# Kernel tuning notes

Measured on AMD Instinct MI355X. Metric: run time of the kernel, lower is better.

Reference implementation:

```python
import jax, jax.numpy as jnp
import numpy as np
from math import sqrt

NUM_HEADS = 16
DIM_MODEL = 1024


def setup_inputs() -> dict:
    key = jax.random.key(0)
    ks = jax.random.split(key, 12)
    B, S, D, M = 4, 1024, DIM_MODEL, 64
    bound = 1.0 / sqrt(D)
    def lin_w(k):
        return jax.random.uniform(k, (D, D), jnp.float32, -bound, bound)
    def lin_b(k):
        return jax.random.uniform(k, (D,), jnp.float32, -bound, bound)
    return {
        "query": jax.random.normal(ks[0], (B, S, D), jnp.float32),
        "key": jax.random.normal(ks[1], (B, S, D), jnp.float32),
        "value": jax.random.normal(ks[2], (B, S, D), jnp.float32),
        "mask": jax.random.randint(ks[3], (1, B, S, M), 0, 2).astype(jnp.float32),
        "Wq": lin_w(ks[4]), "bq": lin_b(ks[5]),
        "Wk": lin_w(ks[6]), "bk": lin_b(ks[7]),
        "Wv": lin_w(ks[8]), "bv": lin_b(ks[9]),
        "Wo": lin_w(ks[10]),
    }


def reference(query, key, value, mask, Wq, bq, Wk, bk, Wv, bv, Wo):
    B, S, D = query.shape
    H = NUM_HEADS
    d = D // H
    # projections + head split, permute(2,0,1,3) -> [H,B,S,d]
    q = (query @ Wq.T + bq).reshape(B, S, H, d).transpose(2, 0, 1, 3)
    k = (key @ Wk.T + bk).reshape(B, S, H, d).transpose(2, 0, 1, 3)
    v = (value @ Wv.T + bv).reshape(B, S, H, d).transpose(2, 0, 1, 3)
    attn = jnp.einsum("hbqd,hbkd->hbqk", q, k) / sqrt(d)  # [H,B,S,S]
    # custom mask: mask.repeat(H,1,1,1) then mask @ mask^T / sqrt(m).
    # Identical per-head, so compute once on [B,S,m] and broadcast over H.
    m2d = mask[0]  # [B,S,m]
    mm = jnp.einsum("bqm,bkm->bqk", m2d, m2d) / sqrt(m2d.shape[-1])
    attn = jnp.where(mm[None] == 0, jnp.float32(-1e9), attn)
    w = jax.nn.softmax(attn, axis=-1)  # dropout is identity in eval mode
    x = jnp.einsum("hbqk,hbkd->hbqd", w, v)  # [H,B,S,d]
    # torch: permute(1,2,0,3) -> [B,S,H,d]; transpose(1,2) -> [B,H,S,d];
    # contiguous().view(B,-1,H*d) -- row-major reshape (mixes head/seq layout, replicated faithfully)
    x = jnp.transpose(x, (1, 0, 2, 3))  # [B,H,S,d]
    x = x.reshape(B, -1, H * d)
    return x @ Wo.T
```

## Files before the change

### kernel.cpp

```cpp
#include <hip/hip_runtime.h>

typedef unsigned int u32;
typedef unsigned short u16;
typedef unsigned long long u64;
typedef __attribute__((ext_vector_type(8))) short s16x8;
typedef __attribute__((ext_vector_type(8))) __bf16 bf16x8;
typedef __attribute__((ext_vector_type(4))) float f32x4;
typedef __attribute__((ext_vector_type(16))) float f32x16;
typedef __attribute__((ext_vector_type(4))) u32 u32x4;

#define WSMB (1ull << 20)
#define QSC 0.18033688011112042f

static __device__ __forceinline__ u16 f2bf(float f) {
  u32 u = __builtin_bit_cast(u32, f);
  return (u16)((u + 0x7fffu + ((u >> 16) & 1u)) >> 16);
}

static __device__ __forceinline__ u32 pkbf(float lo, float hi) {
  u32 r;
  asm("v_cvt_pk_bf16_f32 %0, %1, %2" : "=v"(r) : "v"(lo), "v"(hi));
  return r;
}

static __device__ __forceinline__ float ex2(float x) {
  float r;
  asm("v_exp_f32 %0, %1" : "=v"(r) : "v"(x));
  return r;
}

static __device__ __forceinline__ f32x4 mfma16x16(s16x8 a, s16x8 b, f32x4 c) {
  return __builtin_amdgcn_mfma_f32_16x16x32_bf16(
      __builtin_bit_cast(bf16x8, a), __builtin_bit_cast(bf16x8, b), c, 0, 0, 0);
}

static __device__ __forceinline__ f32x16 mfma32x32(s16x8 a, s16x8 b, f32x16 c) {
  return __builtin_amdgcn_mfma_f32_32x32x16_bf16(
      __builtin_bit_cast(bf16x8, a), __builtin_bit_cast(bf16x8, b), c, 0, 0, 0);
}

#define GLOAD_LDS16(g, l)                                                      \
  __builtin_amdgcn_global_load_lds(                                            \
      (const __attribute__((address_space(1))) u32*)(const void*)(g),          \
      (__attribute__((address_space(3))) u32*)(void*)(l), 16, 0, 0)

__global__ __launch_bounds__(256) void k_prep(
    const float* __restrict__ xq, const float* __restrict__ xk,
    const float* __restrict__ xv, const float* __restrict__ wq,
    const float* __restrict__ wk, const float* __restrict__ wv,
    const float* __restrict__ wo, const float* __restrict__ mask,
    u16* __restrict__ oxq, u16* __restrict__ oxk, u16* __restrict__ oxv,
    u16* __restrict__ owq, u16* __restrict__ owk, u16* __restrict__ owv,
    u16* __restrict__ owo, u64* __restrict__ bits) {
  const int y = blockIdx.y;
  if (y >= 3 && blockIdx.x >= 1024) return;
  if (y == 7) {
    int w = threadIdx.x >> 6, l = threadIdx.x & 63;
    int r = blockIdx.x * 4 + w;
    float v = mask[(size_t)r * 64 + l];
    u64 bl = __ballot(v != 0.0f);
    if (l == 0) bits[r] = bl;
    return;
  }
  const float* s;
  u16* d;
  switch (y) {
    case 0: s = xq; d = oxq; break;
    case 1: s = xk; d = oxk; break;
    case 2: s = xv; d = oxv; break;
    case 3: s = wq; d = owq; break;
    case 4: s = wk; d = owk; break;
    case 5: s = wv; d = owv; break;
    default: s = wo; d = owo; break;
  }
  int i = (blockIdx.x * 256 + threadIdx.x) * 4;
  float4 v = *(const float4*)(s + i);
  u64 p = (u64)f2bf(v.x) | ((u64)f2bf(v.y) << 16) | ((u64)f2bf(v.z) << 32) |
          ((u64)f2bf(v.w) << 48);
  *(u64*)(d + i) = p;
}

__global__ __launch_bounds__(256) void k_mm(const u64* __restrict__ bits,
                                            u64* __restrict__ MB) {
  int wv = threadIdx.x >> 6, l = threadIdx.x & 63;
  int qg = blockIdx.x * 4 + wv;
  u64 bq = bits[qg];
  const u64* bb = bits + (qg & ~1023);
  u64* out = MB + (size_t)qg * 16;
  for (int kt = 0; kt < 16; kt++) {
    u64 bk = bb[kt * 64 + l];
    u64 m = __ballot((bq & bk) != 0ull);
    if (l == 0) out[kt] = m;
  }
}

static __device__ __forceinline__ void gemm_core(const u16* __restrict__ A,
                                                 const u16* __restrict__ Bw,
                                                 f32x4 (&acc)[4][4]) {
  __shared__ __attribute__((aligned(16))) u16 As[2][4096];
  __shared__ __attribute__((aligned(16))) u16 Bs[2][4096];
  const int t = threadIdx.x;
  const int l = t & 63, w = t >> 6, lr = l & 15, lk = l >> 4;
  const int amr = (w & 1) * 64, bnr = (w >> 1) * 64;
  const int c0 = t, c1 = t + 256;
  const int r0 = c0 >> 2, r1 = c1 >> 2;
  const int sw0 = ((c0 & 3) * 8) ^ ((r0 & 6) << 2);
  const int sw1 = ((c1 & 3) * 8) ^ ((r1 & 6) << 2);
  const u16* Ag0 = A + (size_t)r0 * 1024 + sw0;
  const u16* Ag1 = A + (size_t)r1 * 1024 + sw1;
  const u16* Bg0 = Bw + (size_t)r0 * 1024 + sw0;
  const u16* Bg1 = Bw + (size_t)r1 * 1024 + sw1;
  const int aswz = (lk * 16) ^ ((lr & 6) << 3);

  GLOAD_LDS16(Ag0, &As[0][c0 * 8]);
  GLOAD_LDS16(Ag1, &As[0][c1 * 8]);
  GLOAD_LDS16(Bg0, &Bs[0][c0 * 8]);
  GLOAD_LDS16(Bg1, &Bs[0][c1 * 8]);

  int cur = 0;
  for (int kt = 0; kt < 1024; kt += 32) {
    __syncthreads();
    if (kt < 992) {
      const int nxt = cur ^ 1;
      GLOAD_LDS16(Ag0 + kt + 32, &As[nxt][c0 * 8]);
      GLOAD_LDS16(Ag1 + kt + 32, &As[nxt][c1 * 8]);
      GLOAD_LDS16(Bg0 + kt + 32, &Bs[nxt][c0 * 8]);
      GLOAD_LDS16(Bg1 + kt + 32, &Bs[nxt][c1 * 8]);
    }
    const char* Ac = (const char*)As[cur];
    const char* Bc = (const char*)Bs[cur];
    s16x8 af[4], bf[4];
#pragma unroll
    for (int i = 0; i < 4; i++)
      af[i] = *(const s16x8*)(Ac + (amr + i * 16 + lr) * 64 + aswz);
#pragma unroll
    for (int j = 0; j < 4; j++)
      bf[j] = *(const s16x8*)(Bc + (bnr + j * 16 + lr) * 64 + aswz);
    __builtin_amdgcn_s_setprio(1);
#pragma unroll
    for (int i = 0; i < 4; i++)
#pragma unroll
      for (int j = 0; j < 4; j++)
        acc[i][j] = mfma16x16(af[i], bf[j], acc[i][j]);
    __builtin_amdgcn_s_setprio(0);
    cur ^= 1;
  }
}

__global__ __launch_bounds__(256) void k_qkv(
    const u16* __restrict__ Xq, const u16* __restrict__ Xk,
    const u16* __restrict__ Xv, const u16* __restrict__ Wqb,
    const u16* __restrict__ Wkb, const u16* __restrict__ Wvb,
    const float* __restrict__ bq, const float* __restrict__ bk,
    const float* __restrict__ bv, u16* __restrict__ Qo, u16* __restrict__ Ko,
    u16* __restrict__ V4) {
  const int bid0 = blockIdx.x;
  const int bid = (bid0 & 7) * 96 + (bid0 >> 3);
  const int proj = bid >> 8;
  const int rem = bid & 255;
  const int st = rem >> 3, dt = rem & 7;
  const u16* Xp = proj == 0 ? Xq : (proj == 1 ? Xk : Xv);
  const u16* Wp = proj == 0 ? Wqb : (proj == 1 ? Wkb : Wvb);
  const float* bias = proj == 0 ? bq : (proj == 1 ? bk : bv);
  const int t = threadIdx.x;
  const int l = t & 63, w = t >> 6, lr = l & 15, lk = l >> 4;
  const int amr = (w & 1) * 64, bnr = (w >> 1) * 64;
  f32x4 acc[4][4] = {};
  if (proj < 2) {
    const float sc = proj == 0 ? QSC : 1.0f;
    gemm_core(Wp + (size_t)dt * 131072, Xp + (size_t)st * 131072, acc);
    u16* O = proj ? Ko : Qo;
#pragma unroll
    for (int i = 0; i < 4; i++) {
      const int d0 = dt * 128 + amr + i * 16 + lk * 4;
      const int h = d0 >> 6, dd0 = d0 & 63;
      const float4 b4 = *(const float4*)(bias + d0);
#pragma unroll
      for (int j = 0; j < 4; j++) {
        const int s = st * 128 + bnr + j * 16 + lr;
        const int b_ = s >> 10, si = s & 1023;
        u32 e0 = pkbf((acc[i][j][0] + b4.x) * sc, (acc[i][j][1] + b4.y) * sc);
        u32 e1 = pkbf((acc[i][j][2] + b4.z) * sc, (acc[i][j][3] + b4.w) * sc);
        *(u64*)(O + ((size_t)((b_ * 16 + h) * 1024 + si)) * 64 + dd0) =
            (u64)e0 | ((u64)e1 << 32);
      }
    }
  } else {
    gemm_core(Xp + (size_t)st * 131072, Wp + (size_t)dt * 131072, acc);
#pragma unroll
    for (int i = 0; i < 4; i++) {
      const int s0 = st * 128 + amr + i * 16 + lk * 4;
      const int b_ = s0 >> 10, si = s0 & 1023;
      const int sblk = si >> 3, soff = si & 7;
#pragma unroll
      for (int j = 0; j < 4; j++) {
        const int d = dt * 128 + bnr + j * 16 + lr;
        const int h = d >> 6, dd = d & 63;
        const float bb = bias[d];
        u32 e0 = pkbf(acc[i][j][0] + bb, acc[i][j][1] + bb);
        u32 e1 = pkbf(acc[i][j][2] + bb, acc[i][j][3] + bb);
        *(u64*)(V4 + (size_t)(b_ * 16 + h) * 65536 +
                (size_t)(sblk * 64 + dd) * 8 + soff) =
            (u64)e0 | ((u64)e1 << 32);
      }
    }
  }
}

__global__ __launch_bounds__(256) void k_oproj(const u16* __restrict__ Xb,
                                               const u16* __restrict__ Wob,
                                               float* __restrict__ Out) {
  const int bid0 = blockIdx.x;
  const int bid = (bid0 & 7) * 32 + (bid0 >> 3);
  const int mb = bid >> 3, nb = bid & 7;
  f32x4 acc[4][4] = {};
  gemm_core(Xb + (size_t)mb * 131072, Wob + (size_t)nb * 131072, acc);
  const int t = threadIdx.x;
  const int l = t & 63, w = t >> 6, lr = l & 15, lk = l >> 4;
  const int amr = (w & 1) * 64, bnr = (w >> 1) * 64;
#pragma unroll
  for (int i = 0; i < 4; i++)
#pragma unroll
    for (int j = 0; j < 4; j++)
#pragma unroll
      for (int r = 0; r < 4; r++) {
        const int m = mb * 128 + amr + i * 16 + lk * 4 + r;
        const int n = nb * 128 + bnr + j * 16 + lr;
        Out[(size_t)m * 1024 + n] = acc[i][j][r];
      }
}

__global__ __launch_bounds__(256, 3) void k_attn(const u16* __restrict__ Qb,
                                                 const u16* __restrict__ Kb,
                                                 const u16* __restrict__ V4,
                                                 const u64* __restrict__ MB,
                                                 u16* __restrict__ xbuf) {
  __shared__ __attribute__((aligned(16))) u16 Ks[2][4096];
  __shared__ __attribute__((aligned(16))) u16 Vs[2][4096];
  const int t = threadIdx.x, l = t & 63, w = t >> 6;
  const int q5 = l & 31, hi = l >> 5;
  const int bid = (blockIdx.x & 7) * 64 + (blockIdx.x >> 3);
  const int qt = bid & 7, hb = bid >> 3;
  const int h = hb >> 2, b = hb & 3;
  const int s0 = qt * 128;
  const u16* Qhb = Qb + (size_t)(b * 16 + h) * 65536;
  const u16* Khb = Kb + (size_t)(b * 16 + h) * 65536;
  const u16* Vhb = V4 + (size_t)(b * 16 + h) * 65536;
  const int q = s0 + w * 32 + q5;
  const u64* MBq = MB + ((size_t)b * 1024 + q) * 16;

  s16x8 qf[4];
#pragma unroll
  for (int ds = 0; ds < 4; ds++)
    qf[ds] = *(const s16x8*)(Qhb + (size_t)q * 64 + ds * 16 + hi * 8);

  f32x16 xa0 = {}, xa1 = {};
  float ls = 0.f, m_ = -__builtin_inff();

  const int ca = t, cb_ = t + 256;
  const int rA = ca >> 3, colA = (ca & 7) * 16;
  const int rB = cb_ >> 3, colB = (cb_ & 7) * 16;
  const int sA = colA ^ ((rA & 7) << 4);
  const int sB = colB ^ ((rB & 7) << 4);
  const u16* KgA = Khb + (size_t)rA * 64 + (sA >> 1);
  const u16* KgB = Khb + (size_t)rB * 64 + (sB >> 1);
  const u16* VgA = Vhb + (size_t)(sA >> 4) * 512 + rA * 8;
  const u16* VgB = Vhb + (size_t)(sB >> 4) * 512 + rB * 8;

  const int rbase = q5 * 128 + ((hi * 16) ^ ((q5 & 7) << 4));

  GLOAD_LDS16(KgA, &Ks[0][ca * 8]);
  GLOAD_LDS16(KgB, &Ks[0][cb_ * 8]);
  GLOAD_LDS16(VgA, &Vs[0][ca * 8]);
  GLOAD_LDS16(VgB, &Vs[0][cb_ * 8]);
  u64 mw = MBq[0];

  int cur = 0;
  for (int kt = 0; kt < 16; kt++) {
    __syncthreads();
    if (kt < 15) {
      const int nxt = cur ^ 1;
      GLOAD_LDS16(KgA + (kt + 1) * 4096, &Ks[nxt][ca * 8]);
      GLOAD_LDS16(KgB + (kt + 1) * 4096, &Ks[nxt][cb_ * 8]);
      GLOAD_LDS16(VgA + (kt + 1) * 4096, &Vs[nxt][ca * 8]);
      GLOAD_LDS16(VgB + (kt + 1) * 4096, &Vs[nxt][cb_ * 8]);
    }
    const u64 nw = MBq[(kt + 1) & 15];
    const char* Kc = (const char*)Ks[cur];
    const char* Vc = (const char*)Vs[cur];

    f32x16 z0 = {}, z1 = {};
#pragma unroll
    for (int ds = 0; ds < 4; ds++) {
      s16x8 k0 = *(const s16x8*)(Kc + (rbase ^ (ds * 32)));
      s16x8 k1 = *(const s16x8*)(Kc + 4096 + (rbase ^ (ds * 32)));
      __builtin_amdgcn_s_setprio(1);
      z0 = mfma32x32(k0, qf[ds], z0);
      z1 = mfma32x32(k1, qf[ds], z1);
      __builtin_amdgcn_s_setprio(0);
    }

    float tmx[16];
#pragma unroll
    for (int r = 0; r < 16; r++) tmx[r] = fmaxf(z0[r], z1[r]);
#pragma unroll
    for (int st_ = 8; st_ >= 1; st_ >>= 1)
#pragma unroll
      for (int r = 0; r < 8; r++)
        if (r < st_) tmx[r] = fmaxf(tmx[r], tmx[r + st_]);
    float tm = tmx[0];
    tm = fmaxf(tm, __shfl_xor(tm, 32));
    if (tm > m_) {
      const float scl = ex2(m_ - tm);
      m_ = tm;
      ls *= scl;
      xa0 *= scl;
      xa1 *= scl;
    }

    float e0[16], e1[16];
#pragma unroll
    for (int r = 0; r < 16; r++) e0[r] = ex2(z0[r] - m_);
#pragma unroll
    for (int r = 0; r < 16; r++) e1[r] = ex2(z1[r] - m_);
    if (!__all(mw == ~0ull)) {
      const u32 mh0 = (u32)(mw >> (hi * 4));
      const u32 mh1 = (u32)(mw >> (hi * 4 + 32));
#pragma unroll
      for (int r = 0; r < 16; r++) {
        const int bp = 8 * (r >> 2) + (r & 3);
        e0[r] = ((mh0 >> bp) & 1u) ? e0[r] : 0.f;
        e1[r] = ((mh1 >> bp) & 1u) ? e1[r] : 0.f;
      }
    }
    float ts = 0.f;
#pragma unroll
    for (int r = 0; r < 16; r++) ts += e0[r] + e1[r];
    ls += ts;

    u32 P0[2][4], P1[2][4];
#pragma unroll
    for (int qi = 0; qi < 4; qi++) {
      P0[0][qi] = pkbf(e0[4 * qi], e0[4 * qi + 1]);
      P1[0][qi] = pkbf(e0[4 * qi + 2], e0[4 * qi + 3]);
      P0[1][qi] = pkbf(e1[4 * qi], e1[4 * qi + 1]);
      P1[1][qi] = pkbf(e1[4 * qi + 2], e1[4 * qi + 3]);
    }

#pragma unroll
    for (int ks = 0; ks < 4; ks++) {
      const int kb = ks >> 1, qi0 = (ks & 1) * 2, qi1 = qi0 + 1;
      u32 w0 = P0[kb][qi0], w2 = P0[kb][qi1];
      u32 w1 = P1[kb][qi0], w3 = P1[kb][qi1];
      asm("v_permlane32_swap_b32 %0, %1" : "+v"(w0), "+v"(w2));
      asm("v_permlane32_swap_b32 %0, %1" : "+v"(w1), "+v"(w3));
      u32x4 fv;
      fv[0] = w0; fv[1] = w1; fv[2] = w2; fv[3] = w3;
      const s16x8 pb = __builtin_bit_cast(s16x8, fv);
      s16x8 v0 = *(const s16x8*)(Vc + (rbase ^ (ks * 32)));
      s16x8 v1 = *(const s16x8*)(Vc + 4096 + (rbase ^ (ks * 32)));
      __builtin_amdgcn_s_setprio(1);
      xa0 = mfma32x32(v0, pb, xa0);
      xa1 = mfma32x32(v1, pb, xa1);
      __builtin_amdgcn_s_setprio(0);
    }
    mw = nw;
    cur ^= 1;
  }

  ls += __shfl_xor(ls, 32);
  const float inv = 1.0f / ls;
  const size_t rowb = (size_t)b * 1048576 + (size_t)(h * 64 + (q >> 4)) * 1024 +
                      (size_t)(q & 15) * 64;
#pragma unroll
  for (int qi = 0; qi < 4; qi++) {
    u32 a0 = pkbf(xa0[4 * qi] * inv, xa0[4 * qi + 1] * inv);
    u32 a1 = pkbf(xa0[4 * qi + 2] * inv, xa0[4 * qi + 3] * inv);
    *(u64*)(xbuf + rowb + 8 * qi + 4 * hi) = (u64)a0 | ((u64)a1 << 32);
    u32 b0 = pkbf(xa1[4 * qi] * inv, xa1[4 * qi + 1] * inv);
    u32 b1 = pkbf(xa1[4 * qi + 2] * inv, xa1[4 * qi + 3] * inv);
    *(u64*)(xbuf + rowb + 32 + 8 * qi + 4 * hi) = (u64)b0 | ((u64)b1 << 32);
  }
}

extern "C" void kernel_launch(void* const* d_in, const int* in_sizes, int n_in,
                              void* d_out, int out_size, void* d_ws,
                              size_t ws_size, hipStream_t stream) {
  const float* query = (const float*)d_in[0];
  const float* key_ = (const float*)d_in[1];
  const float* value = (const float*)d_in[2];
  const float* mask = (const float*)d_in[3];
  const float* bq = (const float*)d_in[5];
  const float* bk = (const float*)d_in[7];
  const float* bv = (const float*)d_in[9];
  const float* Wq = (const float*)d_in[4];
  const float* Wk = (const float*)d_in[6];
  const float* Wv = (const float*)d_in[8];
  const float* Wo = (const float*)d_in[10];

  char* ws = (char*)d_ws;
  u16* Xq = (u16*)(ws + 0 * WSMB);
  u16* Xk = (u16*)(ws + 8 * WSMB);
  u16* Xv = (u16*)(ws + 16 * WSMB);
  u16* Wqb = (u16*)(ws + 24 * WSMB);
  u16* Wkb = (u16*)(ws + 26 * WSMB);
  u16* Wvb = (u16*)(ws + 28 * WSMB);
  u16* Wob = (u16*)(ws + 30 * WSMB);
  u16* Qb = (u16*)(ws + 32 * WSMB);
  u16* Kb = (u16*)(ws + 40 * WSMB);
  u16* V4 = (u16*)(ws + 48 * WSMB);
  u64* bits = (u64*)(ws + 56 * WSMB);
  u64* MBm = (u64*)(ws + 8 * WSMB);
  u16* xbuf = Xq;

  k_prep<<<dim3(4096, 8), 256, 0, stream>>>(query, key_, value, Wq, Wk, Wv, Wo,
                                            mask, Xq, Xk, Xv, Wqb, Wkb, Wvb,
                                            Wob, bits);
  k_qkv<<<768, 256, 0, stream>>>(Xq, Xk, Xv, Wqb, Wkb, Wvb, bq, bk, bv, Qb, Kb,
                                 V4);
  k_mm<<<1024, 256, 0, stream>>>(bits, MBm);
  k_attn<<<512, 256, 0, stream>>>(Qb, Kb, V4, MBm, xbuf);
  k_oproj<<<256, 256, 0, stream>>>(xbuf, Wob, (float*)d_out);
}
```

Measured before the change: 116.9 us.

## Flatten prep grid, fuse mask-matmul into QKV launch, halve oproj tile width

Replaces the 2D prep grid, which launched many blocks that exited immediately, with a flat 1D grid holding exactly the needed blocks. The mask-bit matmul kernel is folded into the QKV projection launch as extra blocks, which removes one launch and lets that work overlap the GEMM tail. Its output buffer moves to a separate workspace slot so it cannot collide with the bf16 X buffers still being read. The output projection uses 128x64 tiles instead of 128x128, doubling the block count to 512 for better CU occupancy, at the cost of reloading the A operand more often.

```diff
diff --git a/kernel.cpp b/kernel.cpp
--- a/kernel.cpp
+++ b/kernel.cpp
@@ -52,11 +52,10 @@
     u16* __restrict__ oxq, u16* __restrict__ oxk, u16* __restrict__ oxv,
     u16* __restrict__ owq, u16* __restrict__ owk, u16* __restrict__ owv,
     u16* __restrict__ owo, u64* __restrict__ bits) {
-  const int y = blockIdx.y;
-  if (y >= 3 && blockIdx.x >= 1024) return;
-  if (y == 7) {
+  const int bid = blockIdx.x;
+  if (bid >= 16384) {
     int w = threadIdx.x >> 6, l = threadIdx.x & 63;
-    int r = blockIdx.x * 4 + w;
+    int r = (bid - 16384) * 4 + w;
     float v = mask[(size_t)r * 64 + l];
     u64 bl = __ballot(v != 0.0f);
     if (l == 0) bits[r] = bl;
@@ -64,34 +63,26 @@
   }
   const float* s;
   u16* d;
-  switch (y) {
-    case 0: s = xq; d = oxq; break;
-    case 1: s = xk; d = oxk; break;
-    case 2: s = xv; d = oxv; break;
-    case 3: s = wq; d = owq; break;
-    case 4: s = wk; d = owk; break;
-    case 5: s = wv; d = owv; break;
-    default: s = wo; d = owo; break;
-  }
-  int i = (blockIdx.x * 256 + threadIdx.x) * 4;
+  int x;
+  if (bid < 12288) {
+    const int y = bid >> 12;
+    x = bid & 4095;
+    if (y == 0) { s = xq; d = oxq; }
+    else if (y == 1) { s = xk; d = oxk; }
+    else { s = xv; d = oxv; }
+  } else {
+    const int y = (bid - 12288) >> 10;
+    x = (bid - 12288) & 1023;
+    if (y == 0) { s = wq; d = owq; }
+    else if (y == 1) { s = wk; d = owk; }
+    else if (y == 2) { s = wv; d = owv; }
+    else { s = wo; d = owo; }
+  }
+  int i = (x * 256 + threadIdx.x) * 4;
   float4 v = *(const float4*)(s + i);
   u64 p = (u64)f2bf(v.x) | ((u64)f2bf(v.y) << 16) | ((u64)f2bf(v.z) << 32) |
           ((u64)f2bf(v.w) << 48);
   *(u64*)(d + i) = p;
-}
-
-__global__ __launch_bounds__(256) void k_mm(const u64* __restrict__ bits,
-                                            u64* __restrict__ MB) {
-  int wv = threadIdx.x >> 6, l = threadIdx.x & 63;
-  int qg = blockIdx.x * 4 + wv;
-  u64 bq = bits[qg];
-  const u64* bb = bits + (qg & ~1023);
-  u64* out = MB + (size_t)qg * 16;
-  for (int kt = 0; kt < 16; kt++) {
-    u64 bk = bb[kt * 64 + l];
-    u64 m = __ballot((bq & bk) != 0ull);
-    if (l == 0) out[kt] = m;
-  }
 }
 
 static __device__ __forceinline__ void gemm_core(const u16* __restrict__ A,
@@ -147,14 +138,78 @@
   }
 }
 
+static __device__ __forceinline__ void gemm_core64(const u16* __restrict__ A,
+                                                   const u16* __restrict__ Bw,
+                                                   f32x4 (&acc)[4][2]) {
+  __shared__ __attribute__((aligned(16))) u16 As[2][4096];
+  __shared__ __attribute__((aligned(16))) u16 Bs[2][2048];
+  const int t = threadIdx.x;
+  const int l = t & 63, w = t >> 6, lr = l & 15, lk = l >> 4;
+  const int amr = (w & 1) * 64, bnr = (w >> 1) * 32;
+  const int c0 = t, c1 = t + 256;
+  const int r0 = c0 >> 2, r1 = c1 >> 2;
+  const int sw0 = ((c0 & 3) * 8) ^ ((r0 & 6) << 2);
+  const int sw1 = ((c1 & 3) * 8) ^ ((r1 & 6) << 2);
+  const u16* Ag0 = A + (size_t)r0 * 1024 + sw0;
+  const u16* Ag1 = A + (size_t)r1 * 1024 + sw1;
+  const u16* Bg0 = Bw + (size_t)r0 * 1024 + sw0;
+  const int aswz = (lk * 16) ^ ((lr & 6) << 3);
+
+  GLOAD_LDS16(Ag0, &As[0][c0 * 8]);
+  GLOAD_LDS16(Ag1, &As[0][c1 * 8]);
+  GLOAD_LDS16(Bg0, &Bs[0][c0 * 8]);
+
+  int cur = 0;
+  for (int kt = 0; kt < 1024; kt += 32) {
+    __syncthreads();
+    if (kt < 992) {
+      const int nxt = cur ^ 1;
+      GLOAD_LDS16(Ag0 + kt + 32, &As[nxt][c0 * 8]);
+      GLOAD_LDS16(Ag1 + kt + 32, &As[nxt][c1 * 8]);
+      GLOAD_LDS16(Bg0 + kt + 32, &Bs[nxt][c0 * 8]);
+    }
+    const char* Ac = (const char*)As[cur];
+    const char* Bc = (const char*)Bs[cur];
+    s16x8 af[4], bf[2];
+#pragma unroll
+    for (int i = 0; i < 4; i++)
+      af[i] = *(const s16x8*)(Ac + (amr + i * 16 + lr) * 64 + aswz);
+#pragma unroll
+    for (int j = 0; j < 2; j++)
+      bf[j] = *(const s16x8*)(Bc + (bnr + j * 16 + lr) * 64 + aswz);
+    __builtin_amdgcn_s_setprio(1);
+#pragma unroll
+    for (int i = 0; i < 4; i++)
+#pragma unroll
+      for (int j = 0; j < 2; j++)
+        acc[i][j] = mfma16x16(af[i], bf[j], acc[i][j]);
+    __builtin_amdgcn_s_setprio(0);
+    cur ^= 1;
+  }
+}
+
 __global__ __launch_bounds__(256) void k_qkv(
     const u16* __restrict__ Xq, const u16* __restrict__ Xk,
     const u16* __restrict__ Xv, const u16* __restrict__ Wqb,
     const u16* __restrict__ Wkb, const u16* __restrict__ Wvb,
     const float* __restrict__ bq, const float* __restrict__ bk,
     const float* __restrict__ bv, u16* __restrict__ Qo, u16* __restrict__ Ko,
-    u16* __restrict__ V4) {
+    u16* __restrict__ V4, const u64* __restrict__ bits,
+    u64* __restrict__ MB) {
   const int bid0 = blockIdx.x;
+  if (bid0 >= 768) {
+    int wv = threadIdx.x >> 6, l = threadIdx.x & 63;
+    int qg = (bid0 - 768) * 4 + wv;
+    u64 bqw = bits[qg];
+    const u64* bb = bits + (qg & ~1023);
+    u64* out = MB + (size_t)qg * 16;
+    for (int kt = 0; kt < 16; kt++) {
+      u64 bkw = bb[kt * 64 + l];
+      u64 m = __ballot((bqw & bkw) != 0ull);
+      if (l == 0) out[kt] = m;
+    }
+    return;
+  }
   const int bid = (bid0 & 7) * 96 + (bid0 >> 3);
   const int proj = bid >> 8;
   const int rem = bid & 255;
@@ -211,21 +266,21 @@
                                                const u16* __restrict__ Wob,
                                                float* __restrict__ Out) {
   const int bid0 = blockIdx.x;
-  const int bid = (bid0 & 7) * 32 + (bid0 >> 3);
-  const int mb = bid >> 3, nb = bid & 7;
-  f32x4 acc[4][4] = {};
-  gemm_core(Xb + (size_t)mb * 131072, Wob + (size_t)nb * 131072, acc);
+  const int bid = (bid0 & 7) * 64 + (bid0 >> 3);
+  const int mb = bid >> 4, nb = bid & 15;
+  f32x4 acc[4][2] = {};
+  gemm_core64(Xb + (size_t)mb * 131072, Wob + (size_t)nb * 65536, acc);
   const int t = threadIdx.x;
   const int l = t & 63, w = t >> 6, lr = l & 15, lk = l >> 4;
-  const int amr = (w & 1) * 64, bnr = (w >> 1) * 64;
+  const int amr = (w & 1) * 64, bnr = (w >> 1) * 32;
 #pragma unroll
   for (int i = 0; i < 4; i++)
 #pragma unroll
-    for (int j = 0; j < 4; j++)
+    for (int j = 0; j < 2; j++)
 #pragma unroll
       for (int r = 0; r < 4; r++) {
         const int m = mb * 128 + amr + i * 16 + lk * 4 + r;
-        const int n = nb * 128 + bnr + j * 16 + lr;
+        const int n = nb * 64 + bnr + j * 16 + lr;
         Out[(size_t)m * 1024 + n] = acc[i][j][r];
       }
 }
@@ -410,15 +465,13 @@
   u16* Kb = (u16*)(ws + 40 * WSMB);
   u16* V4 = (u16*)(ws + 48 * WSMB);
   u64* bits = (u64*)(ws + 56 * WSMB);
-  u64* MBm = (u64*)(ws + 8 * WSMB);
+  u64* MBm = (u64*)(ws + 57 * WSMB);
   u16* xbuf = Xq;
 
-  k_prep<<<dim3(4096, 8), 256, 0, stream>>>(query, key_, value, Wq, Wk, Wv, Wo,
-                                            mask, Xq, Xk, Xv, Wqb, Wkb, Wvb,
-                                            Wob, bits);
-  k_qkv<<<768, 256, 0, stream>>>(Xq, Xk, Xv, Wqb, Wkb, Wvb, bq, bk, bv, Qb, Kb,
-                                 V4);
-  k_mm<<<1024, 256, 0, stream>>>(bits, MBm);
+  k_prep<<<17408, 256, 0, stream>>>(query, key_, value, Wq, Wk, Wv, Wo, mask,
+                                    Xq, Xk, Xv, Wqb, Wkb, Wvb, Wob, bits);
+  k_qkv<<<1792, 256, 0, stream>>>(Xq, Xk, Xv, Wqb, Wkb, Wvb, bq, bk, bv, Qb,
+                                  Kb, V4, bits, MBm);
   k_attn<<<512, 256, 0, stream>>>(Qb, Kb, V4, MBm, xbuf);
-  k_oproj<<<256, 256, 0, stream>>>(xbuf, Wob, (float*)d_out);
-}
+  k_oproj<<<512, 256, 0, stream>>>(xbuf, Wob, (float*)d_out);
+}
```

After: 114.9 us. About the same (-1.7%).
